# Optimization experiments

Hardware: AMD Instinct MI355X
Metric: run time of the kernel (lower is better)

## Reference

```python
import jax, jax.numpy as jnp
import numpy as np

EPS = 1e-5

def inorm(x, w, b):
    # InstanceNorm1d over token dim (axis=1), per (batch, feature); biased var
    m = x.mean(axis=1, keepdims=True)
    v = ((x - m) ** 2).mean(axis=1, keepdims=True)
    return (x - m) / jnp.sqrt(v + EPS) * w + b

def setup_inputs() -> dict:
    B, N, D, FH = 2, 512, 128, 512
    key = jax.random.key(0)
    ks = iter(jax.random.split(key, 48))
    rn = lambda shape, s=0.05: jax.random.normal(next(ks), shape, jnp.float32) * s
    inp = {
        'row_emb': jax.random.normal(next(ks), (B, N, D), jnp.float32),
        'col_emb': jax.random.normal(next(ks), (B, N, D), jnp.float32),
        'cost_mat': jax.random.uniform(next(ks), (B, N, N), jnp.float32),
        'coords': jax.random.uniform(next(ks), (B, N, 2), jnp.float32),
        'alpha': jnp.ones((1,), jnp.float32),
        # instance norm affine params (weight~1, bias~0)
        'n1_w': 1.0 + rn((D,)), 'n1_b': rn((D,)),
        'n2_w': 1.0 + rn((D,)), 'n2_b': rn((D,)),
        'n3_w': 1.0 + rn((D,)), 'n3_b': rn((D,)),
        'fn1_w': 1.0 + rn((D,)), 'fn1_b': rn((D,)),
        'fn2_w': 1.0 + rn((D,)), 'fn2_b': rn((D,)),
        # AFTFull projections (stored (in,out))
        'q_w': rn((D, D)), 'q_b': rn((D,)),
        'k_w': rn((D, D)), 'k_b': rn((D,)),
        'v_w': rn((D, D)), 'v_b': rn((D,)),
        'p_w': rn((D, D)), 'p_b': rn((D,)),
        'mhc_w': rn((D, D)), 'mhc_b': rn((D,)),
        # DistAngleFusion MLPs
        'dist_w1': rn((1, D)), 'dist_b1': rn((D,)),
        'dist_w2': rn((D, D)), 'dist_b2': rn((D,)),
        'ang_w1': rn((1, D)), 'ang_b1': rn((D,)),
        'ang_w2': rn((D, D)), 'ang_b2': rn((D,)),
        'gate_w': rn((2 * D, 1)), 'gate_b': rn((1,)),
        'outlin_w': rn((D, 1)), 'outlin_b': rn((1,)),
        # FeedForward
        'ffn_w1': rn((D, FH)), 'ffn_b1': rn((FH,)),
        'ffn_w2': rn((FH, D)), 'ffn_b2': rn((D,)),
    }
    return inp

def reference(row_emb, col_emb, cost_mat, coords, alpha,
              n1_w, n1_b, n2_w, n2_b, n3_w, n3_b, fn1_w, fn1_b, fn2_w, fn2_b,
              q_w, q_b, k_w, k_b, v_w, v_b, p_w, p_b, mhc_w, mhc_b,
              dist_w1, dist_b1, dist_w2, dist_b2,
              ang_w1, ang_b1, ang_w2, ang_b2,
              gate_w, gate_b, outlin_w, outlin_b,
              ffn_w1, ffn_b1, ffn_w2, ffn_b2):
    rn = inorm(row_emb, n1_w, n1_b)
    cn = inorm(col_emb, n2_w, n2_b)

    # DistAngleFusion: adapt_bias (B,N,N)
    diff = coords[:, :, None, :] - coords[:, None, :, :]  # (B,N,N,2)
    angles = jnp.arctan2(diff[..., 1], diff[..., 0])
    dist_e = jax.nn.relu(cost_mat[..., None] @ dist_w1 + dist_b1) @ dist_w2 + dist_b2  # (B,N,N,D)
    angle_e = jax.nn.relu(angles[..., None] @ ang_w1 + ang_b1) @ ang_w2 + ang_b2
    g = jax.nn.sigmoid(jnp.concatenate([dist_e, angle_e], axis=-1) @ gate_w + gate_b)  # (B,N,N,1)
    fused = g * dist_e + (1.0 - g) * angle_e
    adapt_bias = (fused @ outlin_w + outlin_b)[..., 0] * alpha  # (B,N,N)

    # AFTFull
    Q = jax.nn.sigmoid(rn @ q_w + q_b)          # (B,N,H)
    K = jax.nn.softmax(cn @ k_w + k_b, axis=1)  # softmax over tokens
    V = cn @ v_w + v_b
    eab = jnp.exp(jax.nn.softmax(adapt_bias, axis=-1))  # (B,N,N)
    eK = jnp.exp(K)
    num = jnp.einsum('bnm,bmh->bnh', eab, eK * V)
    den = jnp.einsum('bnm,bmh->bnh', eab, eK)
    Yt = (Q * (num / den)) @ p_w + p_b

    mh = inorm(Yt @ mhc_w + mhc_b, n3_w, n3_b)

    # TransformerFFN with instance norms
    x = inorm(rn + mh, fn1_w, fn1_b)
    ff = jax.nn.relu(x @ ffn_w1 + ffn_b1) @ ffn_w2 + ffn_b2
    return inorm(x + ff, fn2_w, fn2_b)
```

## Files before the change

kernel.cpp:

```cpp
#include <hip/hip_runtime.h>
#include <hip/hip_bf16.h>
#include <math.h>

#define Bn  2
#define Nn  512
#define Dn  128
#define FHn 512

#define PI_F 3.14159265358979323846f

typedef __hip_bfloat16 bf16;

__device__ __forceinline__ float cvt(float x) { return x; }
__device__ __forceinline__ float cvt(bf16 x) { return __bfloat162float(x); }
__device__ __forceinline__ float sigmoidf_(float x) { return 1.0f / (1.0f + __expf(-x)); }
__device__ __forceinline__ bool is_bf16(const void* alpha) {
    return ((const unsigned short*)alpha)[0] == 0x3F80;
}

__device__ __forceinline__ float fatan2f(float dy, float dx) {
    float ax = fabsf(dx), ay = fabsf(dy);
    float mx = fmaxf(ax, ay), mn = fminf(ax, ay);
    float r = __fdividef(mn, mx);
    float t = r * r;
    float a = r * (0.99997726f + t * (-0.33262347f + t * (0.19354346f +
              t * (-0.11643287f + t * (0.05265332f + t * (-0.01172120f))))));
    if (ay > ax) a = 1.57079632679489662f - a;
    if (dx < 0.f) a = PI_F - a;
    if (dy < 0.f) a = -a;
    return fminf(fmaxf(a, -PI_F), PI_F);
}

#define S_ 131072
#define WS_Q    (0 * S_)
#define WS_K    (1 * S_)
#define WS_V    (2 * S_)
#define WS_MH   (3 * S_)
#define WS_T    (4 * S_)
#define WS_OP   (5 * S_)
#define WS_ST   (6 * S_)

#define ST_IN_SC   0
#define ST_IN_SH   512
#define ST_X_SC    2048
#define ST_X_SH    2304
#define ST_PRE     3072
#define P_SC       1024
#define ST_TAB     4224
#define TAB_ANG 644
#define TAB_N   1288
#define ST_LUTC (ST_TAB + TAB_N)
#define ST_LUTA (ST_LUTC + 257)
#define TABLUT_N (TAB_N + 514)

#define SMEM_FLOATS 2568

struct KP {
    const void *row, *col, *cost, *coords, *alpha;
    const void *n1w, *n1b, *n2w, *n2b, *n3w, *n3b, *f1w, *f1b, *f2w, *f2b;
    const void *qw, *qb, *kw, *kb, *vw, *vb, *pw, *pb, *mw, *mb;
    const void *dw1, *db1, *dw2, *db2, *aw1, *ab1, *aw2, *ab2, *gw, *gb, *ow, *ob;
    const void *ffw1, *ffb1, *ffw2, *ffb2;
    void* out;
    float* ws;
};

__device__ __forceinline__ void blk_sum2(float& s, float& ss, volatile float* scr) {
#pragma unroll
    for (int off = 32; off > 0; off >>= 1) { s += __shfl_down(s, off); ss += __shfl_down(ss, off); }
    __syncthreads();
    int wave = threadIdx.x >> 6, lane = threadIdx.x & 63;
    if (lane == 0) { scr[wave] = s; scr[4 + wave] = ss; }
    __syncthreads();
    s = scr[0] + scr[1] + scr[2] + scr[3];
    ss = scr[4] + scr[5] + scr[6] + scr[7];
}

template <typename T>
__device__ void build_tables(const T* w1p, const T* b1p, const T* w2p,
                             const T* owp, const T* gwp, float* gtab, float* smem) {
    int tid = threadIdx.x;
    float* W  = smem;
    float* Bb = smem + 128;
    float* U  = smem + 256;
    float* Vv = smem + 384;
    float* Tt = smem + 512;
    int* RK   = (int*)(smem + 640);
    float* STl = smem + 768;
    if (tid < 128) {
        float u = 0.f, v = 0.f;
#pragma unroll 4
        for (int d = 0; d < Dn; ++d) {
            float w2 = cvt(w2p[tid * Dn + d]);
            u += w2 * cvt(owp[d]);
            v += w2 * cvt(gwp[d]);
        }
        float w = cvt(w1p[tid]), b = cvt(b1p[tid]);
        U[tid] = u; Vv[tid] = v; W[tid] = w; Bb[tid] = b;
        Tt[tid] = (w != 0.f) ? (-b / w) : 3.0e38f;
    }
    __syncthreads();
    if (tid < 128) {
        float tk = Tt[tid]; int r = 0;
        for (int j = 0; j < 128; ++j) {
            float tj = Tt[j];
            r += (tj < tk) || (tj == tk && j < tid);
        }
        RK[tid] = r;
        gtab[r] = tk;
        STl[r] = tk;
    }
    __syncthreads();
    if (tid <= 128) {
        int si = tid;
        float slS = 0, inS = 0, slT = 0, inT = 0;
        for (int k = 0; k < 128; ++k) {
            float w = W[k];
            if (w == 0.f) {
                float rb = fmaxf(Bb[k], 0.f);
                inS += rb * U[k];
                inT += rb * Vv[k];
            } else {
                bool act = (w > 0.f) ? (RK[k] < si) : (RK[k] >= si);
                if (act) {
                    slS += w * U[k];  inS += Bb[k] * U[k];
                    slT += w * Vv[k]; inT += Bb[k] * Vv[k];
                }
            }
        }
        gtab[128 + si] = slS;
        gtab[257 + si] = inS;
        gtab[386 + si] = slT;
        gtab[515 + si] = inT;
    }
}

__device__ __forceinline__ int bsearch128(const float* T, float c) {
    int lo = 0, hi = 128;
    while (lo < hi) { int mid = (lo + hi) >> 1; if (T[mid] <= c) lo = mid + 1; else hi = mid; }
    return lo;
}

template <typename T>
__device__ void phase0(const KP& p, float* st, float* smem) {
    float* scr = smem + 2560;
    int cid = blockIdx.x;
    int tid = threadIdx.x;
    {
        int which = cid >> 8, b = (cid >> 7) & 1, d = cid & 127;
        const T* src = (const T*)(which ? p.col : p.row) + (size_t)b * Nn * Dn + d;
        float x0 = cvt(src[(size_t)tid * Dn]);
        float x1 = cvt(src[(size_t)(tid + 256) * Dn]);
        float s = x0 + x1, ss = x0 * x0 + x1 * x1;
        blk_sum2(s, ss, scr);
        if (tid == 0) {
            float m = s * (1.f / Nn);
            float v = fmaxf(ss * (1.f / Nn) - m * m, 0.f);
            float rstd = rsqrtf(v + 1e-5f);
            const T* w = which ? (const T*)p.n2w : (const T*)p.n1w;
            const T* bb = which ? (const T*)p.n2b : (const T*)p.n1b;
            float sc = rstd * cvt(w[d]);
            st[ST_IN_SC + cid] = sc;
            st[ST_IN_SH + cid] = cvt(bb[d]) - m * sc;
        }
    }
    __syncthreads();
    if (cid == 128) {
        const T* db2 = (const T*)p.db2; const T* ab2 = (const T*)p.ab2;
        const T* ow = (const T*)p.ow;   const T* gw = (const T*)p.gw;
        float d2 = 0.f, a2 = 0.f, o = 0.f, g0 = 0.f, g1 = 0.f;
        if (tid < 128) {
            d2 = cvt(db2[tid]); a2 = cvt(ab2[tid]);
            o = cvt(ow[tid]); g0 = cvt(gw[tid]); g1 = cvt(gw[Dn + tid]);
        }
        float cds = d2 * o, cdt = d2 * g0, cas = a2 * o, cat = a2 * g1;
        blk_sum2(cds, cdt, scr);
        blk_sum2(cas, cat, scr);
        if (tid == 0) {
            float* pre = st + ST_PRE;
            pre[P_SC + 0] = cds; pre[P_SC + 1] = cdt;
            pre[P_SC + 2] = cas; pre[P_SC + 3] = cat;
            pre[P_SC + 4] = cvt(((const T*)p.gb)[0]);
            pre[P_SC + 5] = cvt(((const T*)p.ob)[0]);
            pre[P_SC + 6] = cvt(((const T*)p.alpha)[0]);
        }
    } else if (cid == 129) {
        build_tables<T>((const T*)p.dw1, (const T*)p.db1, (const T*)p.dw2,
                        (const T*)p.ow, (const T*)p.gw, st + ST_TAB, smem);
        __syncthreads();
        const float* STl = smem + 768;
        for (int e = tid; e < 257; e += 256) {
            float c = e * (1.f / 256.f);
            st[ST_LUTC + e] = (float)bsearch128(STl, c);
        }
    } else if (cid == 130) {
        build_tables<T>((const T*)p.aw1, (const T*)p.ab1, (const T*)p.aw2,
                        (const T*)p.ow, (const T*)p.gw + Dn, st + ST_TAB + TAB_ANG, smem);
        __syncthreads();
        const float* STl = smem + 768;
        for (int e = tid; e < 257; e += 256) {
            float a = -PI_F + e * (PI_F / 128.f);
            st[ST_LUTA + e] = (float)bsearch128(STl, a);
        }
    }
}

template <typename T>
__device__ void phase1(const KP& p, float* st, float* smem) {
    int tid = threadIdx.x;
    int r0 = blockIdx.x * 4;
    int b = r0 >> 9;
    const T* row = (const T*)p.row; const T* col = (const T*)p.col;
    float* ws = p.ws;
    float* Q = ws + WS_Q; float* Kraw = ws + WS_K; float* V = ws + WS_V;

    float* lr = smem;
    float* lc = smem + 512;
    float* redq = smem + 1024;
    float* redk = smem + 3072;
    float* redv = smem + 5120;
    {
        int r = tid >> 7, d = tid & 127;
        float scR = st[ST_IN_SC + b * 128 + d],       shR = st[ST_IN_SH + b * 128 + d];
        float scC = st[ST_IN_SC + 256 + b * 128 + d], shC = st[ST_IN_SH + 256 + b * 128 + d];
        lr[r * 128 + d] = cvt(row[(size_t)(r0 + r) * Dn + d]) * scR + shR;
        lc[r * 128 + d] = cvt(col[(size_t)(r0 + r) * Dn + d]) * scC + shC;
    }
    __syncthreads();
    {
        int h = tid & 127, q = tid >> 7;
        const T* qw = (const T*)p.qw; const T* kw = (const T*)p.kw; const T* vw = (const T*)p.vw;
        float aq[4] = {0,0,0,0}, ak[4] = {0,0,0,0}, av[4] = {0,0,0,0};
        int ks = q * 32;
#pragma unroll 8
        for (int k = ks; k < ks + 32; ++k) {
            float wq = cvt(qw[k * Dn + h]);
            float wk = cvt(kw[k * Dn + h]);
            float wv = cvt(vw[k * Dn + h]);
#pragma unroll
            for (int r = 0; r < 4; ++r) {
                aq[r] += lr[r * 128 + k] * wq;
                ak[r] += lc[r * 128 + k] * wk;
                av[r] += lc[r * 128 + k] * wv;
            }
        }
#pragma unroll
        for (int r = 0; r < 4; ++r) {
            redq[q * 512 + r * 128 + h] = aq[r];
            redk[q * 512 + r * 128 + h] = ak[r];
            redv[q * 512 + r * 128 + h] = av[r];
        }
    }
    __syncthreads();
    if (tid < 128) {
        int h = tid;
        float bq = cvt(((const T*)p.qb)[h]);
        float bk = cvt(((const T*)p.kb)[h]);
        float bv = cvt(((const T*)p.vb)[h]);
#pragma unroll
        for (int r = 0; r < 4; ++r) {
            float qv = redq[r*128+h] + redq[512 + r*128+h] + redq[1024 + r*128+h] + redq[1536 + r*128+h] + bq;
            float kv = redk[r*128+h] + redk[512 + r*128+h] + redk[1024 + r*128+h] + redk[1536 + r*128+h] + bk;
            float vv = redv[r*128+h] + redv[512 + r*128+h] + redv[1024 + r*128+h] + redv[1536 + r*128+h] + bv;
            Q[(r0 + r) * Dn + h]    = sigmoidf_(qv);
            Kraw[(r0 + r) * Dn + h] = kv;
            V[(r0 + r) * Dn + h]    = vv;
        }
    }
}

template <typename T>
__device__ void phase3(const KP& p, float* st, float* smem) {
    int tid = threadIdx.x;
    int r0 = blockIdx.x * 4;
    int b = r0 >> 9;
    float* ws = p.ws;
    const float* Kraw = ws + WS_K;
    const float* V = ws + WS_V;
    const float* Q = ws + WS_Q;
    float* mh = ws + WS_MH;

    float* ab   = smem;
    float* redn = smem + 2048;
    float* redd = smem + 4096;
    float* gl   = smem + 6144;
    float* yl   = smem + 6656;
    float* scr  = smem + 7168;

    {
        float* tab  = smem + 2048;
        float* lutc = smem + 3336;
        float* luta = smem + 3593;
        const float* gt = st + ST_TAB;
        for (int e = tid; e < TABLUT_N; e += 512) tab[e] = gt[e];
        __syncthreads();
        const float* pre = st + ST_PRE;
        float cds = pre[P_SC + 0], cdt = pre[P_SC + 1], cas = pre[P_SC + 2], cat = pre[P_SC + 3];
        float gbias = pre[P_SC + 4], obias = pre[P_SC + 5], alpha = pre[P_SC + 6];
        const T* cost = (const T*)p.cost;
        const T* coords = (const T*)p.coords;
        const float* tabA = tab + TAB_ANG;

        int j = tid;
        float cjx = cvt(coords[((size_t)b * Nn + j) * 2 + 0]);
        float cjy = cvt(coords[((size_t)b * Nn + j) * 2 + 1]);
        float av[4];
#pragma unroll
        for (int rr = 0; rr < 4; ++rr) {
            int i = (r0 + rr) & 511;
            float cix = cvt(coords[((size_t)b * Nn + i) * 2 + 0]);
            float ciy = cvt(coords[((size_t)b * Nn + i) * 2 + 1]);
            float c = cvt(cost[(size_t)b * Nn * Nn + (size_t)i * Nn + j]);
            int k = (int)(c * 256.f); k = k < 0 ? 0 : (k > 255 ? 255 : k);
            int lo = (int)lutc[k], hi = (int)lutc[k + 1];
            while (lo < hi && tab[lo] <= c) ++lo;
            float sd = fmaf(tab[128 + lo], c, tab[257 + lo]) + cds;
            float td = fmaf(tab[386 + lo], c, tab[515 + lo]) + cdt;
            float dx = cix - cjx;
            float dy = ciy - cjy;
            float ang = (dx == 0.f && dy == 0.f) ? 0.f : fatan2f(dy, dx);
            int ka = (int)((ang + PI_F) * (128.f / PI_F)); ka = ka < 0 ? 0 : (ka > 255 ? 255 : ka);
            int la = (int)luta[ka], ha = (int)luta[ka + 1];
            while (la < ha && tabA[la] <= ang) ++la;
            float sa = fmaf(tabA[128 + la], ang, tabA[257 + la]) + cas;
            float ta = fmaf(tabA[386 + la], ang, tabA[515 + la]) + cat;
            float gv = sigmoidf_(td + ta + gbias);
            av[rr] = alpha * (gv * sd + (1.f - gv) * sa + obias);
        }
        int wave = tid >> 6, lane = tid & 63;
        float t0 = av[0], t1 = av[1], t2 = av[2], t3 = av[3];
#pragma unroll
        for (int off = 32; off > 0; off >>= 1) {
            t0 = fmaxf(t0, __shfl_down(t0, off));
            t1 = fmaxf(t1, __shfl_down(t1, off));
            t2 = fmaxf(t2, __shfl_down(t2, off));
            t3 = fmaxf(t3, __shfl_down(t3, off));
        }
        __syncthreads();
        if (lane == 0) { scr[wave] = t0; scr[8 + wave] = t1; scr[16 + wave] = t2; scr[24 + wave] = t3; }
        __syncthreads();
        float mx[4], ev[4];
#pragma unroll
        for (int rr = 0; rr < 4; ++rr) {
            float m = scr[rr * 8];
#pragma unroll
            for (int w = 1; w < 8; ++w) m = fmaxf(m, scr[rr * 8 + w]);
            mx[rr] = m;
            ev[rr] = __expf(av[rr] - m);
        }
        float s0 = ev[0], s1 = ev[1], s2 = ev[2], s3 = ev[3];
#pragma unroll
        for (int off = 32; off > 0; off >>= 1) {
            s0 += __shfl_down(s0, off);
            s1 += __shfl_down(s1, off);
            s2 += __shfl_down(s2, off);
            s3 += __shfl_down(s3, off);
        }
        if (lane == 0) { scr[32 + wave] = s0; scr[40 + wave] = s1; scr[48 + wave] = s2; scr[56 + wave] = s3; }
        __syncthreads();
#pragma unroll
        for (int rr = 0; rr < 4; ++rr) {
            float s = 0.f;
#pragma unroll
            for (int w = 0; w < 8; ++w) s += scr[32 + rr * 8 + w];
            ab[rr * 512 + j] = __expf(ev[rr] / s);
        }
    }
    __syncthreads();

    int h = tid & 127, q = tid >> 7;
    const float* kbase = Kraw + (size_t)b * Nn * Dn + h;
    const float* vbase = V + (size_t)b * Nn * Dn + h;
    int j0 = q * 128;

    float mxk, rsk;
    {
        float lm = -3.0e38f;
        for (int j = j0; j < j0 + 128; ++j) lm = fmaxf(lm, kbase[(size_t)j * Dn]);
        redn[q * 128 + h] = lm;
        __syncthreads();
        mxk = fmaxf(fmaxf(redn[h], redn[128 + h]), fmaxf(redn[256 + h], redn[384 + h]));
        float ls = 0.f;
        for (int j = j0; j < j0 + 128; ++j) ls += __expf(kbase[(size_t)j * Dn] - mxk);
        redd[q * 128 + h] = ls;
        __syncthreads();
        rsk = 1.f / (redd[h] + redd[128 + h] + redd[256 + h] + redd[384 + h]);
    }
    __syncthreads();

    {
        float num[4] = {0,0,0,0}, den[4] = {0,0,0,0};
#pragma unroll 4
        for (int j = j0; j < j0 + 128; ++j) {
            float kv_ = kbase[(size_t)j * Dn];
            float ek = __expf(__expf(kv_ - mxk) * rsk);
            float ev_ = ek * vbase[(size_t)j * Dn];
#pragma unroll
            for (int r = 0; r < 4; ++r) {
                num[r] += ab[r * 512 + j] * ev_;
                den[r] += ab[r * 512 + j] * ek;
            }
        }
#pragma unroll
        for (int r = 0; r < 4; ++r) {
            redn[q * 512 + r * 128 + h] = num[r];
            redd[q * 512 + r * 128 + h] = den[r];
        }
    }
    __syncthreads();
    if (tid < 128) {
#pragma unroll
        for (int r = 0; r < 4; ++r) {
            float nu = redn[r * 128 + h] + redn[512 + r * 128 + h]
                     + redn[1024 + r * 128 + h] + redn[1536 + r * 128 + h];
            float de = redd[r * 128 + h] + redd[512 + r * 128 + h]
                     + redd[1024 + r * 128 + h] + redd[1536 + r * 128 + h];
            gl[r * 128 + h] = Q[(r0 + r) * Dn + h] * nu / de;
        }
    }
    __syncthreads();
    {
        const T* pw = (const T*)p.pw;
        float acc[4] = {0,0,0,0};
        int ks = q * 32;
#pragma unroll 8
        for (int k = ks; k < ks + 32; ++k) {
            float w = cvt(pw[k * Dn + h]);
#pragma unroll
            for (int r = 0; r < 4; ++r) acc[r] += gl[r * 128 + k] * w;
        }
#pragma unroll
        for (int r = 0; r < 4; ++r) redn[q * 512 + r * 128 + h] = acc[r];
    }
    __syncthreads();
    if (tid < 128) {
        float bp = cvt(((const T*)p.pb)[h]);
#pragma unroll
        for (int r = 0; r < 4; ++r)
            yl[r * 128 + h] = redn[r * 128 + h] + redn[512 + r * 128 + h]
                            + redn[1024 + r * 128 + h] + redn[1536 + r * 128 + h] + bp;
    }
    __syncthreads();
    {
        const T* mw = (const T*)p.mw;
        float acc[4] = {0,0,0,0};
        int ks = q * 32;
#pragma unroll 8
        for (int k = ks; k < ks + 32; ++k) {
            float w = cvt(mw[k * Dn + h]);
#pragma unroll
            for (int r = 0; r < 4; ++r) acc[r] += yl[r * 128 + k] * w;
        }
#pragma unroll
        for (int r = 0; r < 4; ++r) redn[q * 512 + r * 128 + h] = acc[r];
    }
    __syncthreads();
    if (tid < 128) {
        float bm = cvt(((const T*)p.mb)[h]);
#pragma unroll
        for (int r = 0; r < 4; ++r)
            mh[(r0 + r) * Dn + h] = redn[r * 128 + h] + redn[512 + r * 128 + h]
                                  + redn[1024 + r * 128 + h] + redn[1536 + r * 128 + h] + bm;
    }
}

template <typename T>
__device__ void phase45(const KP& p, float* st, float* smem) {
    float* scr = smem + 2560;
    int tid = threadIdx.x;
    int c = blockIdx.x;
    int b = c >> 7, d = c & 127;
    const float* mh = p.ws + WS_MH;
    const float* mp = mh + (size_t)b * Nn * Dn + d;
    float m0 = mp[(size_t)tid * Dn], m1 = mp[(size_t)(tid + 256) * Dn];
    float s = m0 + m1, ss = m0 * m0 + m1 * m1;
    blk_sum2(s, ss, scr);
    float mm = s * (1.f / Nn);
    float vv = fmaxf(ss * (1.f / Nn) - mm * mm, 0.f);
    float rstd = rsqrtf(vv + 1e-5f);
    float scM = rstd * cvt(((const T*)p.n3w)[d]);
    float shM = cvt(((const T*)p.n3b)[d]) - mm * scM;
    const T* row = (const T*)p.row;
    float scI = st[ST_IN_SC + c], shI = st[ST_IN_SH + c];
    const T* rp = row + (size_t)b * Nn * Dn + d;
    float* tp = p.ws + WS_T + (size_t)b * Nn * Dn + d;
    float x0 = cvt(rp[(size_t)tid * Dn]) * scI + shI + m0 * scM + shM;
    float x1 = cvt(rp[(size_t)(tid + 256) * Dn]) * scI + shI + m1 * scM + shM;
    tp[(size_t)tid * Dn] = x0;
    tp[(size_t)(tid + 256) * Dn] = x1;
    __syncthreads();
    float s2 = x0 + x1, ss2 = x0 * x0 + x1 * x1;
    blk_sum2(s2, ss2, scr);
    if (tid == 0) {
        float m = s2 * (1.f / Nn);
        float v = fmaxf(ss2 * (1.f / Nn) - m * m, 0.f);
        float r = rsqrtf(v + 1e-5f);
        float sc = r * cvt(((const T*)p.f1w)[d]);
        st[ST_X_SC + c] = sc;
        st[ST_X_SH + c] = cvt(((const T*)p.f1b)[d]) - m * sc;
    }
}

template <typename T>
__device__ void phase6(const KP& p, float* st, float* smem) {
    int tid = threadIdx.x;
    int r0 = blockIdx.x * 4;
    int b = r0 >> 9;
    const float* t = p.ws + WS_T;
    float* outpre = p.ws + WS_OP;
    const T* w1 = (const T*)p.ffw1; const T* b1 = (const T*)p.ffb1;
    const T* w2 = (const T*)p.ffw2; const T* b2 = (const T*)p.ffb2;

    float* xl = smem;
    float* hl = smem + 512;
    float* red = smem + 2560;
    {
        int r = tid >> 7, d = tid & 127;
        int c = b * 128 + d;
        xl[r * 128 + d] = t[(r0 + r) * Dn + d] * st[ST_X_SC + c] + st[ST_X_SH + c];
    }
    __syncthreads();
    {
        int f = tid;
        float a[4] = {0,0,0,0};
#pragma unroll 4
        for (int k = 0; k < Dn; ++k) {
            float w = cvt(w1[k * FHn + f]);
#pragma unroll
            for (int r = 0; r < 4; ++r) a[r] += xl[r * 128 + k] * w;
        }
        float bb1 = cvt(b1[f]);
#pragma unroll
        for (int r = 0; r < 4; ++r) hl[r * 512 + f] = fmaxf(a[r] + bb1, 0.f);
    }
    __syncthreads();
    {
        int d = tid & 127, q = tid >> 7;
        int k0 = q * 128;
        float a[4] = {0,0,0,0};
#pragma unroll 8
        for (int k = k0; k < k0 + 128; ++k) {
            float w = cvt(w2[k * Dn + d]);
#pragma unroll
            for (int r = 0; r < 4; ++r) a[r] += hl[r * 512 + k] * w;
        }
#pragma unroll
        for (int r = 0; r < 4; ++r) red[q * 512 + r * 128 + d] = a[r];
    }
    __syncthreads();
    if (tid < 128) {
        float bb2 = cvt(b2[tid]);
#pragma unroll
        for (int r = 0; r < 4; ++r) {
            float sum = red[r * 128 + tid] + red[512 + r * 128 + tid]
                      + red[1024 + r * 128 + tid] + red[1536 + r * 128 + tid];
            outpre[(r0 + r) * Dn + tid] = xl[r * 128 + tid] + sum + bb2;
        }
    }
}

template <typename T>
__device__ void phase78(const KP& p, float* smem) {
    float* scr = smem + 2560;
    int tid = threadIdx.x;
    int c = blockIdx.x;
    int b = c >> 7, d = c & 127;
    const float* op = p.ws + WS_OP;
    const float* sp = op + (size_t)b * Nn * Dn + d;
    float x0 = sp[(size_t)tid * Dn], x1 = sp[(size_t)(tid + 256) * Dn];
    float s = x0 + x1, ss = x0 * x0 + x1 * x1;
    blk_sum2(s, ss, scr);
    float m = s * (1.f / Nn);
    float v = fmaxf(ss * (1.f / Nn) - m * m, 0.f);
    float rstd = rsqrtf(v + 1e-5f);
    float sc = rstd * cvt(((const T*)p.f2w)[d]);
    float sh = cvt(((const T*)p.f2b)[d]) - m * sc;
    T* out = (T*)p.out + (size_t)b * Nn * Dn + d;
    out[(size_t)tid * Dn] = (T)(x0 * sc + sh);
    out[(size_t)(tid + 256) * Dn] = (T)(x1 * sc + sh);
}

#define PH_WRAP(name, call_bf, call_f)                                        \
__global__ __launch_bounds__(256) void name(KP p) {                           \
    __shared__ float smem[SMEM_FLOATS];                                       \
    float* st = p.ws + WS_ST; (void)st;                                       \
    if (is_bf16(p.alpha)) { call_bf; } else { call_f; }                       \
}

PH_WRAP(k_head,  phase0<bf16>(p, st, smem),  phase0<float>(p, st, smem))
__global__ __launch_bounds__(512) void k_qkv(KP p) {
    __shared__ float smem[7168];
    float* st = p.ws + WS_ST;
    if (is_bf16(p.alpha)) phase1<bf16>(p, st, smem);
    else                  phase1<float>(p, st, smem);
}
__global__ __launch_bounds__(512) void k_attn(KP p) {
    __shared__ float smem[7232];
    float* st = p.ws + WS_ST;
    if (is_bf16(p.alpha)) phase3<bf16>(p, st, smem);
    else                  phase3<float>(p, st, smem);
}
PH_WRAP(k_mid,   phase45<bf16>(p, st, smem), phase45<float>(p, st, smem))
__global__ __launch_bounds__(512) void k_ffn(KP p) {
    __shared__ float smem[4608];
    float* st = p.ws + WS_ST;
    if (is_bf16(p.alpha)) phase6<bf16>(p, st, smem);
    else                  phase6<float>(p, st, smem);
}
PH_WRAP(k_tail,  phase78<bf16>(p, smem),     phase78<float>(p, smem))

extern "C" void kernel_launch(void* const* d_in, const int* in_sizes, int n_in,
                              void* d_out, int out_size, void* d_ws, size_t ws_size,
                              hipStream_t stream) {
    KP p;
    p.row = d_in[0];  p.col = d_in[1];  p.cost = d_in[2];  p.coords = d_in[3];
    p.alpha = d_in[4];
    p.n1w = d_in[5];  p.n1b = d_in[6];  p.n2w = d_in[7];  p.n2b = d_in[8];
    p.n3w = d_in[9];  p.n3b = d_in[10]; p.f1w = d_in[11]; p.f1b = d_in[12];
    p.f2w = d_in[13]; p.f2b = d_in[14];
    p.qw = d_in[15];  p.qb = d_in[16];  p.kw = d_in[17];  p.kb = d_in[18];
    p.vw = d_in[19];  p.vb = d_in[20];  p.pw = d_in[21];  p.pb = d_in[22];
    p.mw = d_in[23];  p.mb = d_in[24];
    p.dw1 = d_in[25]; p.db1 = d_in[26]; p.dw2 = d_in[27]; p.db2 = d_in[28];
    p.aw1 = d_in[29]; p.ab1 = d_in[30]; p.aw2 = d_in[31]; p.ab2 = d_in[32];
    p.gw = d_in[33];  p.gb = d_in[34];  p.ow = d_in[35];  p.ob = d_in[36];
    p.ffw1 = d_in[37]; p.ffb1 = d_in[38]; p.ffw2 = d_in[39]; p.ffb2 = d_in[40];
    p.out = d_out;
    p.ws = (float*)d_ws;

    k_head<<<512, 256, 0, stream>>>(p);
    k_qkv<<<256, 512, 0, stream>>>(p);
    k_attn<<<256, 512, 0, stream>>>(p);
    k_mid<<<256, 256, 0, stream>>>(p);
    k_ffn<<<256, 512, 0, stream>>>(p);
    k_tail<<<256, 256, 0, stream>>>(p);
}
```

Baseline: 253.3 us.

## Precompute K softmax, exp(K) and exp(K)*V in separate kernel before attention

Adds a new kernel that computes the token-axis softmax of K once per (batch, feature) column and stores exp(K) and exp(K)*V in workspace. The attention kernel then reads these directly instead of each of its 256 blocks recomputing column max, sum and double exponentials over 512 tokens. This removes redundant per-block reductions and transcendental work. It costs an extra launch and extra workspace writes and reads, and the workspace layout grows by two slices.

```diff
diff --git a/kernel.cpp b/kernel.cpp
--- a/kernel.cpp
+++ b/kernel.cpp
@@ -35,10 +35,12 @@
 #define WS_Q    (0 * S_)
 #define WS_K    (1 * S_)
 #define WS_V    (2 * S_)
-#define WS_MH   (3 * S_)
-#define WS_T    (4 * S_)
-#define WS_OP   (5 * S_)
-#define WS_ST   (6 * S_)
+#define WS_EK   (3 * S_)
+#define WS_EKV  (4 * S_)
+#define WS_MH   (5 * S_)
+#define WS_T    (6 * S_)
+#define WS_OP   (7 * S_)
+#define WS_ST   (8 * S_)
 
 #define ST_IN_SC   0
 #define ST_IN_SH   512
@@ -74,6 +76,26 @@
     __syncthreads();
     s = scr[0] + scr[1] + scr[2] + scr[3];
     ss = scr[4] + scr[5] + scr[6] + scr[7];
+}
+
+__device__ __forceinline__ float blk_sum1(float v, volatile float* scr) {
+#pragma unroll
+    for (int off = 32; off > 0; off >>= 1) v += __shfl_down(v, off);
+    __syncthreads();
+    int wave = threadIdx.x >> 6, lane = threadIdx.x & 63;
+    if (lane == 0) scr[wave] = v;
+    __syncthreads();
+    return scr[0] + scr[1] + scr[2] + scr[3];
+}
+
+__device__ __forceinline__ float blk_max1(float v, volatile float* scr) {
+#pragma unroll
+    for (int off = 32; off > 0; off >>= 1) v = fmaxf(v, __shfl_down(v, off));
+    __syncthreads();
+    int wave = threadIdx.x >> 6, lane = threadIdx.x & 63;
+    if (lane == 0) scr[wave] = v;
+    __syncthreads();
+    return fmaxf(fmaxf(scr[0], scr[1]), fmaxf(scr[2], scr[3]));
 }
 
 template <typename T>
@@ -269,14 +291,39 @@
     }
 }
 
+__device__ void phase2(const KP& p, float* smem) {
+    float* scr = smem + 2560;
+    int tid = threadIdx.x;
+    int c = blockIdx.x;
+    int b = c >> 7, h = c & 127;
+    float* ws = p.ws;
+    const float* Kraw = ws + WS_K;
+    const float* V = ws + WS_V;
+    float* eK = ws + WS_EK;
+    float* eKV = ws + WS_EKV;
+    const float* kb = Kraw + (size_t)b * Nn * Dn + h;
+    const float* vb = V + (size_t)b * Nn * Dn + h;
+    float x0 = kb[(size_t)tid * Dn];
+    float x1 = kb[(size_t)(tid + 256) * Dn];
+    float mx = blk_max1(fmaxf(x0, x1), scr);
+    float e0 = __expf(x0 - mx), e1 = __expf(x1 - mx);
+    float s = blk_sum1(e0 + e1, scr);
+    float rs = 1.f / s;
+    size_t a0 = (size_t)b * Nn * Dn + (size_t)tid * Dn + h;
+    size_t a1 = (size_t)b * Nn * Dn + (size_t)(tid + 256) * Dn + h;
+    float ek0 = __expf(e0 * rs), ek1 = __expf(e1 * rs);
+    eK[a0] = ek0;  eKV[a0] = ek0 * vb[(size_t)tid * Dn];
+    eK[a1] = ek1;  eKV[a1] = ek1 * vb[(size_t)(tid + 256) * Dn];
+}
+
 template <typename T>
 __device__ void phase3(const KP& p, float* st, float* smem) {
     int tid = threadIdx.x;
     int r0 = blockIdx.x * 4;
     int b = r0 >> 9;
     float* ws = p.ws;
-    const float* Kraw = ws + WS_K;
-    const float* V = ws + WS_V;
+    const float* eK = ws + WS_EK;
+    const float* eKV = ws + WS_EKV;
     const float* Q = ws + WS_Q;
     float* mh = ws + WS_MH;
 
@@ -339,13 +386,12 @@
         __syncthreads();
         if (lane == 0) { scr[wave] = t0; scr[8 + wave] = t1; scr[16 + wave] = t2; scr[24 + wave] = t3; }
         __syncthreads();
-        float mx[4], ev[4];
+        float ev[4];
 #pragma unroll
         for (int rr = 0; rr < 4; ++rr) {
             float m = scr[rr * 8];
 #pragma unroll
             for (int w = 1; w < 8; ++w) m = fmaxf(m, scr[rr * 8 + w]);
-            mx[rr] = m;
             ev[rr] = __expf(av[rr] - m);
         }
         float s0 = ev[0], s1 = ev[1], s2 = ev[2], s3 = ev[3];
@@ -369,32 +415,16 @@
     __syncthreads();
 
     int h = tid & 127, q = tid >> 7;
-    const float* kbase = Kraw + (size_t)b * Nn * Dn + h;
-    const float* vbase = V + (size_t)b * Nn * Dn + h;
     int j0 = q * 128;
 
-    float mxk, rsk;
-    {
-        float lm = -3.0e38f;
-        for (int j = j0; j < j0 + 128; ++j) lm = fmaxf(lm, kbase[(size_t)j * Dn]);
-        redn[q * 128 + h] = lm;
-        __syncthreads();
-        mxk = fmaxf(fmaxf(redn[h], redn[128 + h]), fmaxf(redn[256 + h], redn[384 + h]));
-        float ls = 0.f;
-        for (int j = j0; j < j0 + 128; ++j) ls += __expf(kbase[(size_t)j * Dn] - mxk);
-        redd[q * 128 + h] = ls;
-        __syncthreads();
-        rsk = 1.f / (redd[h] + redd[128 + h] + redd[256 + h] + redd[384 + h]);
-    }
-    __syncthreads();
-
-    {
+    {
+        const float* ekb = eK + (size_t)b * Nn * Dn + h;
+        const float* evb = eKV + (size_t)b * Nn * Dn + h;
         float num[4] = {0,0,0,0}, den[4] = {0,0,0,0};
 #pragma unroll 4
         for (int j = j0; j < j0 + 128; ++j) {
-            float kv_ = kbase[(size_t)j * Dn];
-            float ek = __expf(__expf(kv_ - mxk) * rsk);
-            float ev_ = ek * vbase[(size_t)j * Dn];
+            float ek = ekb[(size_t)j * Dn];
+            float ev_ = evb[(size_t)j * Dn];
 #pragma unroll
             for (int r = 0; r < 4; ++r) {
                 num[r] += ab[r * 512 + j] * ev_;
@@ -594,6 +624,10 @@
     if (is_bf16(p.alpha)) phase1<bf16>(p, st, smem);
     else                  phase1<float>(p, st, smem);
 }
+__global__ __launch_bounds__(256) void k_kekv(KP p) {
+    __shared__ float smem[SMEM_FLOATS];
+    phase2(p, smem);
+}
 __global__ __launch_bounds__(512) void k_attn(KP p) {
     __shared__ float smem[7232];
     float* st = p.ws + WS_ST;
@@ -630,6 +664,7 @@
 
     k_head<<<512, 256, 0, stream>>>(p);
     k_qkv<<<256, 512, 0, stream>>>(p);
+    k_kekv<<<256, 256, 0, stream>>>(p);
     k_attn<<<256, 512, 0, stream>>>(p);
     k_mid<<<256, 256, 0, stream>>>(p);
     k_ffn<<<256, 512, 0, stream>>>(p);
```

Result: faster. 231.5 us (-8.6%).
